# Kernel optimization log

Hardware: AMD Instinct MI355X
Metric: run time of the kernel (lower is better)

The kernel has to match this reference:

```python
import jax, jax.numpy as jnp
import numpy as np


def setup_inputs() -> dict:
    key = jax.random.key(0)
    k1, k2 = jax.random.split(key)
    inputs = jax.random.normal(k1, (16, 64, 64, 64), dtype=jnp.float32)  # NCHW, C=embedding_dim
    codebook = jax.random.normal(k2, (1024, 64), dtype=jnp.float32)      # [K, D]
    return {"inputs": inputs, "codebook": codebook}


def reference(inputs, codebook):
    # inputs: [B, C, H, W] -> [B, H, W, C] -> [N, D]
    D = codebook.shape[1]
    x = jnp.transpose(inputs, (0, 2, 3, 1)).reshape(-1, D)  # [N, D]
    distances = (
        jnp.sum(x * x, axis=1, keepdims=True)
        + jnp.sum(codebook * codebook, axis=1)
        - 2.0 * jnp.matmul(x, codebook.T)
    )
    encoding_indices = jnp.argmin(distances, axis=1)[:, None]  # [N, 1]
    return encoding_indices
```

## Files before the change

kernel.cpp:

```cpp
#include <hip/hip_runtime.h>


typedef float f4 __attribute__((ext_vector_type(4)));
typedef short s8v __attribute__((ext_vector_type(8)));
typedef unsigned int u32;

#define D_DIM 64
#define HW    4096
#define ROWS  64
#define INF_  __builtin_inff()
#define MFMA(a,b,c) __builtin_amdgcn_mfma_f32_16x16x32_bf16(a,b,c,0,0,0)

__device__ __forceinline__ unsigned short bf_rne(float f) {
    u32 u = __builtin_bit_cast(u32, f);
    u32 r = u + 0x7fffu + ((u >> 16) & 1u);
    return (unsigned short)(r >> 16);
}
__device__ __forceinline__ float bf_to_f(unsigned short h) {
    u32 u = ((u32)h) << 16;
    return __builtin_bit_cast(float, u);
}
__device__ __forceinline__ void split3(float f, unsigned short& h,
                                       unsigned short& m, unsigned short& l) {
    h = bf_rne(f);
    float f1 = f - bf_to_f(h);
    m = bf_rne(f1);
    float f2 = f1 - bf_to_f(m);
    l = bf_rne(f2);
}
__device__ __forceinline__ s8v pack8(unsigned short a0, unsigned short a1,
                                     unsigned short a2, unsigned short a3,
                                     unsigned short a4, unsigned short a5,
                                     unsigned short a6, unsigned short a7) {
    uint4 u;
    u.x = a0 | ((u32)a1 << 16);
    u.y = a2 | ((u32)a3 << 16);
    u.z = a4 | ((u32)a5 << 16);
    u.w = a6 | ((u32)a7 << 16);
    return __builtin_bit_cast(s8v, u);
}

__global__ __launch_bounds__(64) void prep_kernel(const float* __restrict__ cb,
                                                  char* __restrict__ wsb) {
    const int blk = blockIdx.x;
    const int lane = threadIdx.x;
    if (blk < 384) {
        const int T = blk / 6;
        const int rem = blk - T * 6;
        const int s = rem / 3;
        const int L = rem - s * 3;
        const int code = T * 16 + (lane & 15);
        const int ch0 = s * 32 + (lane >> 4) * 8;
        const float* src = cb + code * 64 + ch0;
        unsigned short o[8];
#pragma unroll
        for (int j = 0; j < 8; ++j) {
            unsigned short h, m2, l;
            split3(src[j], h, m2, l);
            o[j] = (L == 0) ? h : (L == 1) ? m2 : l;
        }
        uint4 w;
        w.x = o[0] | ((u32)o[1] << 16);
        w.y = o[2] | ((u32)o[3] << 16);
        w.z = o[4] | ((u32)o[5] << 16);
        w.w = o[6] | ((u32)o[7] << 16);
        *(uint4*)(wsb + (size_t)blk * 1024 + lane * 16) = w;
    } else {
        const int k = (blk - 384) * 64 + lane;
        const f4* row = (const f4*)(cb + (size_t)k * 64);
        float sacc = 0.f;
#pragma unroll
        for (int i = 0; i < 16; ++i) {
            f4 v = row[i];
            sacc = fmaf(v.x, v.x, sacc);
            sacc = fmaf(v.y, v.y, sacc);
            sacc = fmaf(v.z, v.z, sacc);
            sacc = fmaf(v.w, v.w, sacc);
        }
        ((float*)(wsb + 384 * 1024))[k] = sacc;
    }
}

#define BUILD_AS(rs, s) {                                                    \
    const float* xr = (const float*)&xs4[(rs) * 16 + m_][0];                 \
    f4 va = *(const f4*)(xr + (s) * 32 + ko);                                \
    f4 vb = *(const f4*)(xr + (s) * 32 + ko + 4);                            \
    unsigned short h0,h1,h2,h3,h4,h5,h6,h7;                                  \
    unsigned short q0,q1,q2,q3,q4,q5,q6,q7;                                  \
    unsigned short l0,l1,l2,l3,l4,l5,l6,l7;                                  \
    split3(-2.f * va.x, h0, q0, l0); split3(-2.f * va.y, h1, q1, l1);        \
    split3(-2.f * va.z, h2, q2, l2); split3(-2.f * va.w, h3, q3, l3);        \
    split3(-2.f * vb.x, h4, q4, l4); split3(-2.f * vb.y, h5, q5, l5);        \
    split3(-2.f * vb.z, h6, q6, l6); split3(-2.f * vb.w, h7, q7, l7);        \
    Ah##rs##s = pack8(h0,h1,h2,h3,h4,h5,h6,h7);                              \
    Am##rs##s = pack8(q0,q1,q2,q3,q4,q5,q6,q7);                              \
    Al##rs##s = pack8(l0,l1,l2,l3,l4,l5,l6,l7);                              \
}

#define LOADB(S, P)                                                          \
    Bh0##S = *(const s8v*)((P) + 0);    Bm0##S = *(const s8v*)((P) + 1024);  \
    Bl0##S = *(const s8v*)((P) + 2048); Bh1##S = *(const s8v*)((P) + 3072);  \
    Bm1##S = *(const s8v*)((P) + 4096); Bl1##S = *(const s8v*)((P) + 5120);

#define MFMA_S(s, BH, BM, BL)                                                \
    acc0 = MFMA(Ah0##s, BH, acc0); acc1 = MFMA(Ah1##s, BH, acc1);            \
    acc2 = MFMA(Ah2##s, BH, acc2); acc3 = MFMA(Ah3##s, BH, acc3);            \
    acc0 = MFMA(Ah0##s, BM, acc0); acc1 = MFMA(Ah1##s, BM, acc1);            \
    acc2 = MFMA(Ah2##s, BM, acc2); acc3 = MFMA(Ah3##s, BM, acc3);            \
    acc0 = MFMA(Am0##s, BH, acc0); acc1 = MFMA(Am1##s, BH, acc1);            \
    acc2 = MFMA(Am2##s, BH, acc2); acc3 = MFMA(Am3##s, BH, acc3);            \
    acc0 = MFMA(Ah0##s, BL, acc0); acc1 = MFMA(Ah1##s, BL, acc1);            \
    acc2 = MFMA(Ah2##s, BL, acc2); acc3 = MFMA(Ah3##s, BL, acc3);            \
    acc0 = MFMA(Am0##s, BM, acc0); acc1 = MFMA(Am1##s, BM, acc1);            \
    acc2 = MFMA(Am2##s, BM, acc2); acc3 = MFMA(Am3##s, BM, acc3);            \
    acc0 = MFMA(Al0##s, BH, acc0); acc1 = MFMA(Al1##s, BH, acc1);            \
    acc2 = MFMA(Al2##s, BH, acc2); acc3 = MFMA(Al3##s, BH, acc3);

#define UPD(rs, i) {                                                         \
    float v = acc##rs[i] + en;                                               \
    bool p = (v < best_##rs##_##i);                                          \
    best_##rs##_##i = p ? v : best_##rs##_##i;                               \
    idx_##rs##_##i  = p ? kn : idx_##rs##_##i;                               \
}
#define EPILOG(TG) {                                                         \
    const int kn = (TG) * 16 + m_;                                           \
    const float en = sEn[kn];                                                \
    UPD(0,0) UPD(0,1) UPD(0,2) UPD(0,3)                                      \
    UPD(1,0) UPD(1,1) UPD(1,2) UPD(1,3)                                      \
    UPD(2,0) UPD(2,1) UPD(2,2) UPD(2,3)                                      \
    UPD(3,0) UPD(3,1) UPD(3,2) UPD(3,3)                                      \
    acc0 = (f4){0.f,0.f,0.f,0.f}; acc1 = (f4){0.f,0.f,0.f,0.f};              \
    acc2 = (f4){0.f,0.f,0.f,0.f}; acc3 = (f4){0.f,0.f,0.f,0.f};              \
}

#define DO_TILE(CUR, NXT, TG, NP) {                                          \
    LOADB(NXT, NP)                                                           \
    MFMA_S(0, Bh0##CUR, Bm0##CUR, Bl0##CUR)                                  \
    MFMA_S(1, Bh1##CUR, Bm1##CUR, Bl1##CUR)                                  \
    EPILOG(TG)                                                               \
}

#define BFLY1(rs, i, msk) {                                                  \
    float ov = __shfl_xor(best_##rs##_##i, msk);                             \
    int   oi = __shfl_xor(idx_##rs##_##i,  msk);                             \
    bool p = (ov < best_##rs##_##i) ||                                       \
             (ov == best_##rs##_##i && oi < idx_##rs##_##i);                 \
    best_##rs##_##i = p ? ov : best_##rs##_##i;                              \
    idx_##rs##_##i  = p ? oi : idx_##rs##_##i;                               \
}
#define BFLY_ALL(msk)                                                        \
    BFLY1(0,0,msk) BFLY1(0,1,msk) BFLY1(0,2,msk) BFLY1(0,3,msk)              \
    BFLY1(1,0,msk) BFLY1(1,1,msk) BFLY1(1,2,msk) BFLY1(1,3,msk)              \
    BFLY1(2,0,msk) BFLY1(2,1,msk) BFLY1(2,2,msk) BFLY1(2,3,msk)              \
    BFLY1(3,0,msk) BFLY1(3,1,msk) BFLY1(3,2,msk) BFLY1(3,3,msk)

#define STORE1(rs, i)                                                        \
    sdq[quarter][(rs) * 16 + rbase + (i)] = best_##rs##_##i;                 \
    siq[quarter][(rs) * 16 + rbase + (i)] = idx_##rs##_##i;

__global__ __launch_bounds__(256, 2) void vq_kernel(const float* __restrict__ x,
                                                    const char* __restrict__ wsb,
                                                    int* __restrict__ out) {
    __shared__ f4    xs4[ROWS][17];
    __shared__ float sEn[1024];
    __shared__ float sdq[4][64];
    __shared__ int   siq[4][64];

    const int tid = threadIdx.x;
    const int lane = tid & 63;
    const int quarter = __builtin_amdgcn_readfirstlane(tid >> 6);
    const int m_ = lane & 15;
    const int ko = (lane >> 4) * 8;
    const int n0 = blockIdx.x * ROWS;
    const int b = n0 >> 12;
    const int hw0 = n0 & (HW - 1);

    const float* enp = (const float*)(wsb + 384 * 1024);
#pragma unroll
    for (int q = 0; q < 4; ++q) sEn[q * 256 + tid] = enp[q * 256 + tid];

    {
        const float* g = x + ((size_t)b * D_DIM + quarter * 16) * HW + hw0 + lane;
        float v[16];
#pragma unroll
        for (int i = 0; i < 16; ++i) v[i] = g[(size_t)i * HW];
#pragma unroll
        for (int j = 0; j < 4; ++j)
            xs4[lane][quarter * 4 + j] = (f4){v[4*j], v[4*j+1], v[4*j+2], v[4*j+3]};
    }
    __syncthreads();

    s8v Ah00, Am00, Al00, Ah01, Am01, Al01;
    s8v Ah10, Am10, Al10, Ah11, Am11, Al11;
    s8v Ah20, Am20, Al20, Ah21, Am21, Al21;
    s8v Ah30, Am30, Al30, Ah31, Am31, Al31;
    BUILD_AS(0,0) BUILD_AS(0,1) BUILD_AS(1,0) BUILD_AS(1,1)
    BUILD_AS(2,0) BUILD_AS(2,1) BUILD_AS(3,0) BUILD_AS(3,1)

    f4 acc0 = (f4){0.f,0.f,0.f,0.f}, acc1 = (f4){0.f,0.f,0.f,0.f};
    f4 acc2 = (f4){0.f,0.f,0.f,0.f}, acc3 = (f4){0.f,0.f,0.f,0.f};
    float best_0_0=INF_, best_0_1=INF_, best_0_2=INF_, best_0_3=INF_;
    float best_1_0=INF_, best_1_1=INF_, best_1_2=INF_, best_1_3=INF_;
    float best_2_0=INF_, best_2_1=INF_, best_2_2=INF_, best_2_3=INF_;
    float best_3_0=INF_, best_3_1=INF_, best_3_2=INF_, best_3_3=INF_;
    int idx_0_0=0, idx_0_1=0, idx_0_2=0, idx_0_3=0;
    int idx_1_0=0, idx_1_1=0, idx_1_2=0, idx_1_3=0;
    int idx_2_0=0, idx_2_1=0, idx_2_2=0, idx_2_3=0;
    int idx_3_0=0, idx_3_1=0, idx_3_2=0, idx_3_3=0;

    s8v Bh0c, Bm0c, Bl0c, Bh1c, Bm1c, Bl1c;
    s8v Bh0n, Bm0n, Bl0n, Bh1n, Bm1n, Bl1n;

    const char* const bp0 = wsb + (size_t)quarter * 98304 + (size_t)lane * 16;
    const char* bp = bp0;
    LOADB(c, bp)
    bp += 6144;

#pragma unroll 1
    for (int tt = 0; tt < 8; ++tt) {
        const int t0 = 2 * tt;
        DO_TILE(c, n, quarter * 16 + t0, bp)
        bp += 6144;
        const char* np = (tt == 7) ? bp0 : bp;
        DO_TILE(n, c, quarter * 16 + t0 + 1, np)
        bp += 6144;
    }

    BFLY_ALL(1) BFLY_ALL(2) BFLY_ALL(4) BFLY_ALL(8)

    if ((lane & 15) == 0) {
        const int rbase = (lane >> 4) * 4;
        STORE1(0,0) STORE1(0,1) STORE1(0,2) STORE1(0,3)
        STORE1(1,0) STORE1(1,1) STORE1(1,2) STORE1(1,3)
        STORE1(2,0) STORE1(2,1) STORE1(2,2) STORE1(2,3)
        STORE1(3,0) STORE1(3,1) STORE1(3,2) STORE1(3,3)
    }
    __syncthreads();

    if (tid < 64) {
        float bv = sdq[0][tid];
        int   bi = siq[0][tid];
#pragma unroll
        for (int q = 1; q < 4; ++q) {
            const float o = sdq[q][tid];
            const int  oi = siq[q][tid];
            if (o < bv) { bv = o; bi = oi; }
        }
        out[n0 + tid] = bi;
    }
}

extern "C" void kernel_launch(void* const* d_in, const int* in_sizes, int n_in,
                              void* d_out, int out_size, void* d_ws, size_t ws_size,
                              hipStream_t stream) {
    const float* x  = (const float*)d_in[0];
    const float* cb = (const float*)d_in[1];
    char* wsb = (char*)d_ws;
    int*  out = (int*)d_out;

    prep_kernel<<<dim3(400), dim3(64), 0, stream>>>(cb, wsb);
    vq_kernel<<<dim3(65536 / ROWS), dim3(256), 0, stream>>>(x, wsb, out);
}
```

Measured before the change: 110.4 us.

## Split rows across waves and stream codebook tiles through LDS with async loads

Each workgroup now handles 128 rows, and each wave owns 32 rows and scans the full codebook, instead of each wave owning a quarter of the codes for 64 shared rows. Codebook split tiles are staged into double-buffered LDS with global_load_lds, shared by all four waves, and synchronised with barriers. This removes the cross-wave argmin merge and cuts global B traffic per row. The costs are two barriers per tile and a serial dependency on the accumulators, since each accumulator now carries a chain of six MFMAs with only four independent chains. The grid is also halved.

Measured after the change: 110.6 us. About the same (+0.2%).

```diff
diff --git a/kernel.cpp b/kernel.cpp
--- a/kernel.cpp
+++ b/kernel.cpp
@@ -4,10 +4,12 @@
 typedef float f4 __attribute__((ext_vector_type(4)));
 typedef short s8v __attribute__((ext_vector_type(8)));
 typedef unsigned int u32;
+typedef __attribute__((address_space(1))) const u32* gas1;
+typedef __attribute__((address_space(3))) u32* las3;
 
 #define D_DIM 64
 #define HW    4096
-#define ROWS  64
+#define ROWS  128
 #define INF_  __builtin_inff()
 #define MFMA(a,b,c) __builtin_amdgcn_mfma_f32_16x16x32_bf16(a,b,c,0,0,0)
 
@@ -38,6 +40,9 @@
     u.z = a4 | ((u32)a5 << 16);
     u.w = a6 | ((u32)a7 << 16);
     return __builtin_bit_cast(s8v, u);
+}
+__device__ __forceinline__ void gl_lds16(const char* g, char* l) {
+    __builtin_amdgcn_global_load_lds((gas1)(const void*)g, (las3)(void*)l, 16, 0, 0);
 }
 
 __global__ __launch_bounds__(64) void prep_kernel(const float* __restrict__ cb,
@@ -82,7 +87,7 @@
 }
 
 #define BUILD_AS(rs, s) {                                                    \
-    const float* xr = (const float*)&xs4[(rs) * 16 + m_][0];                 \
+    const float* xr = (const float*)&xs4[wrow + (rs) * 16 + m_][0];          \
     f4 va = *(const f4*)(xr + (s) * 32 + ko);                                \
     f4 vb = *(const f4*)(xr + (s) * 32 + ko + 4);                            \
     unsigned short h0,h1,h2,h3,h4,h5,h6,h7;                                  \
@@ -97,47 +102,44 @@
     Al##rs##s = pack8(l0,l1,l2,l3,l4,l5,l6,l7);                              \
 }
 
-#define LOADB(S, P)                                                          \
-    Bh0##S = *(const s8v*)((P) + 0);    Bm0##S = *(const s8v*)((P) + 1024);  \
-    Bl0##S = *(const s8v*)((P) + 2048); Bh1##S = *(const s8v*)((P) + 3072);  \
-    Bm1##S = *(const s8v*)((P) + 4096); Bl1##S = *(const s8v*)((P) + 5120);
-
-#define MFMA_S(s, BH, BM, BL)                                                \
-    acc0 = MFMA(Ah0##s, BH, acc0); acc1 = MFMA(Ah1##s, BH, acc1);            \
-    acc2 = MFMA(Ah2##s, BH, acc2); acc3 = MFMA(Ah3##s, BH, acc3);            \
-    acc0 = MFMA(Ah0##s, BM, acc0); acc1 = MFMA(Ah1##s, BM, acc1);            \
-    acc2 = MFMA(Ah2##s, BM, acc2); acc3 = MFMA(Ah3##s, BM, acc3);            \
-    acc0 = MFMA(Am0##s, BH, acc0); acc1 = MFMA(Am1##s, BH, acc1);            \
-    acc2 = MFMA(Am2##s, BH, acc2); acc3 = MFMA(Am3##s, BH, acc3);            \
-    acc0 = MFMA(Ah0##s, BL, acc0); acc1 = MFMA(Ah1##s, BL, acc1);            \
-    acc2 = MFMA(Ah2##s, BL, acc2); acc3 = MFMA(Ah3##s, BL, acc3);            \
-    acc0 = MFMA(Am0##s, BM, acc0); acc1 = MFMA(Am1##s, BM, acc1);            \
-    acc2 = MFMA(Am2##s, BM, acc2); acc3 = MFMA(Am3##s, BM, acc3);            \
-    acc0 = MFMA(Al0##s, BH, acc0); acc1 = MFMA(Al1##s, BH, acc1);            \
-    acc2 = MFMA(Al2##s, BH, acc2); acc3 = MFMA(Al3##s, BH, acc3);
-
-#define UPD(rs, i) {                                                         \
-    float v = acc##rs[i] + en;                                               \
+#define STAGE(T, BUF) {                                                      \
+    const char* gs = wsb + (size_t)(T) * 6144 + lane16;                      \
+    gl_lds16(gs + quarter * 1024, (BUF) + quarter * 1024);                   \
+    if (quarter < 2)                                                         \
+        gl_lds16(gs + (4 + quarter) * 1024, (BUF) + (4 + quarter) * 1024);   \
+}
+
+#define READ6(LP)                                                            \
+    Bh0 = *(const s8v*)((LP) + 0);    Bm0 = *(const s8v*)((LP) + 1024);      \
+    Bl0 = *(const s8v*)((LP) + 2048); Bh1 = *(const s8v*)((LP) + 3072);      \
+    Bm1 = *(const s8v*)((LP) + 4096); Bl1 = *(const s8v*)((LP) + 5120);
+
+#define MTERM(AH, AM, AL, BH, BM, BL, ACC)                                   \
+    ACC = MFMA(AH, BH, ACC); ACC = MFMA(AH, BM, ACC);                        \
+    ACC = MFMA(AM, BH, ACC); ACC = MFMA(AH, BL, ACC);                        \
+    ACC = MFMA(AM, BM, ACC); ACC = MFMA(AL, BH, ACC);
+
+#define COMPUTE24()                                                          \
+    MTERM(Ah00, Am00, Al00, Bh0, Bm0, Bl0, a00)                              \
+    MTERM(Ah10, Am10, Al10, Bh0, Bm0, Bl0, a10)                              \
+    MTERM(Ah01, Am01, Al01, Bh1, Bm1, Bl1, a01)                              \
+    MTERM(Ah11, Am11, Al11, Bh1, Bm1, Bl1, a11)
+
+#define UPD(rs, i, SV) {                                                     \
+    float v = SV[i] + en;                                                    \
     bool p = (v < best_##rs##_##i);                                          \
     best_##rs##_##i = p ? v : best_##rs##_##i;                               \
     idx_##rs##_##i  = p ? kn : idx_##rs##_##i;                               \
 }
-#define EPILOG(TG) {                                                         \
-    const int kn = (TG) * 16 + m_;                                           \
+#define EPILOG(T) {                                                          \
+    const int kn = (T) * 16 + m_;                                            \
     const float en = sEn[kn];                                                \
-    UPD(0,0) UPD(0,1) UPD(0,2) UPD(0,3)                                      \
-    UPD(1,0) UPD(1,1) UPD(1,2) UPD(1,3)                                      \
-    UPD(2,0) UPD(2,1) UPD(2,2) UPD(2,3)                                      \
-    UPD(3,0) UPD(3,1) UPD(3,2) UPD(3,3)                                      \
-    acc0 = (f4){0.f,0.f,0.f,0.f}; acc1 = (f4){0.f,0.f,0.f,0.f};              \
-    acc2 = (f4){0.f,0.f,0.f,0.f}; acc3 = (f4){0.f,0.f,0.f,0.f};              \
-}
-
-#define DO_TILE(CUR, NXT, TG, NP) {                                          \
-    LOADB(NXT, NP)                                                           \
-    MFMA_S(0, Bh0##CUR, Bm0##CUR, Bl0##CUR)                                  \
-    MFMA_S(1, Bh1##CUR, Bm1##CUR, Bl1##CUR)                                  \
-    EPILOG(TG)                                                               \
+    f4 s0 = a00 + a01;                                                       \
+    f4 s1 = a10 + a11;                                                       \
+    UPD(0,0,s0) UPD(0,1,s0) UPD(0,2,s0) UPD(0,3,s0)                          \
+    UPD(1,0,s1) UPD(1,1,s1) UPD(1,2,s1) UPD(1,3,s1)                          \
+    a00 = (f4){0.f,0.f,0.f,0.f}; a01 = (f4){0.f,0.f,0.f,0.f};                \
+    a10 = (f4){0.f,0.f,0.f,0.f}; a11 = (f4){0.f,0.f,0.f,0.f};                \
 }
 
 #define BFLY1(rs, i, msk) {                                                  \
@@ -150,103 +152,93 @@
 }
 #define BFLY_ALL(msk)                                                        \
     BFLY1(0,0,msk) BFLY1(0,1,msk) BFLY1(0,2,msk) BFLY1(0,3,msk)              \
-    BFLY1(1,0,msk) BFLY1(1,1,msk) BFLY1(1,2,msk) BFLY1(1,3,msk)              \
-    BFLY1(2,0,msk) BFLY1(2,1,msk) BFLY1(2,2,msk) BFLY1(2,3,msk)              \
-    BFLY1(3,0,msk) BFLY1(3,1,msk) BFLY1(3,2,msk) BFLY1(3,3,msk)
-
-#define STORE1(rs, i)                                                        \
-    sdq[quarter][(rs) * 16 + rbase + (i)] = best_##rs##_##i;                 \
-    siq[quarter][(rs) * 16 + rbase + (i)] = idx_##rs##_##i;
+    BFLY1(1,0,msk) BFLY1(1,1,msk) BFLY1(1,2,msk) BFLY1(1,3,msk)
 
 __global__ __launch_bounds__(256, 2) void vq_kernel(const float* __restrict__ x,
                                                     const char* __restrict__ wsb,
                                                     int* __restrict__ out) {
-    __shared__ f4    xs4[ROWS][17];
+    __shared__ __align__(16) char LDSA[34816];
     __shared__ float sEn[1024];
-    __shared__ float sdq[4][64];
-    __shared__ int   siq[4][64];
 
     const int tid = threadIdx.x;
     const int lane = tid & 63;
     const int quarter = __builtin_amdgcn_readfirstlane(tid >> 6);
     const int m_ = lane & 15;
     const int ko = (lane >> 4) * 8;
+    const int lane16 = lane * 16;
+    const int wrow = quarter * 32;
     const int n0 = blockIdx.x * ROWS;
     const int b = n0 >> 12;
     const int hw0 = n0 & (HW - 1);
 
+    f4 (*xs4)[17] = (f4(*)[17])(void*)LDSA;
+    char* const buf0 = LDSA;
+    char* const buf1 = LDSA + 6144;
+
     const float* enp = (const float*)(wsb + 384 * 1024);
 #pragma unroll
     for (int q = 0; q < 4; ++q) sEn[q * 256 + tid] = enp[q * 256 + tid];
 
-    {
-        const float* g = x + ((size_t)b * D_DIM + quarter * 16) * HW + hw0 + lane;
+#pragma unroll
+    for (int pass = 0; pass < 2; ++pass) {
+        const int row = lane + pass * 64;
+        const float* g = x + ((size_t)b * D_DIM + quarter * 16) * HW + hw0 + row;
         float v[16];
 #pragma unroll
         for (int i = 0; i < 16; ++i) v[i] = g[(size_t)i * HW];
 #pragma unroll
         for (int j = 0; j < 4; ++j)
-            xs4[lane][quarter * 4 + j] = (f4){v[4*j], v[4*j+1], v[4*j+2], v[4*j+3]};
+            xs4[row][quarter * 4 + j] = (f4){v[4*j], v[4*j+1], v[4*j+2], v[4*j+3]};
     }
     __syncthreads();
 
     s8v Ah00, Am00, Al00, Ah01, Am01, Al01;
     s8v Ah10, Am10, Al10, Ah11, Am11, Al11;
-    s8v Ah20, Am20, Al20, Ah21, Am21, Al21;
-    s8v Ah30, Am30, Al30, Ah31, Am31, Al31;
     BUILD_AS(0,0) BUILD_AS(0,1) BUILD_AS(1,0) BUILD_AS(1,1)
-    BUILD_AS(2,0) BUILD_AS(2,1) BUILD_AS(3,0) BUILD_AS(3,1)
-
-    f4 acc0 = (f4){0.f,0.f,0.f,0.f}, acc1 = (f4){0.f,0.f,0.f,0.f};
-    f4 acc2 = (f4){0.f,0.f,0.f,0.f}, acc3 = (f4){0.f,0.f,0.f,0.f};
+    __syncthreads();
+
+    f4 a00 = (f4){0.f,0.f,0.f,0.f}, a01 = (f4){0.f,0.f,0.f,0.f};
+    f4 a10 = (f4){0.f,0.f,0.f,0.f}, a11 = (f4){0.f,0.f,0.f,0.f};
     float best_0_0=INF_, best_0_1=INF_, best_0_2=INF_, best_0_3=INF_;
     float best_1_0=INF_, best_1_1=INF_, best_1_2=INF_, best_1_3=INF_;
-    float best_2_0=INF_, best_2_1=INF_, best_2_2=INF_, best_2_3=INF_;
-    float best_3_0=INF_, best_3_1=INF_, best_3_2=INF_, best_3_3=INF_;
     int idx_0_0=0, idx_0_1=0, idx_0_2=0, idx_0_3=0;
     int idx_1_0=0, idx_1_1=0, idx_1_2=0, idx_1_3=0;
-    int idx_2_0=0, idx_2_1=0, idx_2_2=0, idx_2_3=0;
-    int idx_3_0=0, idx_3_1=0, idx_3_2=0, idx_3_3=0;
-
-    s8v Bh0c, Bm0c, Bl0c, Bh1c, Bm1c, Bl1c;
-    s8v Bh0n, Bm0n, Bl0n, Bh1n, Bm1n, Bl1n;
-
-    const char* const bp0 = wsb + (size_t)quarter * 98304 + (size_t)lane * 16;
-    const char* bp = bp0;
-    LOADB(c, bp)
-    bp += 6144;
+
+    s8v Bh0, Bm0, Bl0, Bh1, Bm1, Bl1;
+
+    STAGE(0, buf0)
+    __syncthreads();
 
 #pragma unroll 1
-    for (int tt = 0; tt < 8; ++tt) {
-        const int t0 = 2 * tt;
-        DO_TILE(c, n, quarter * 16 + t0, bp)
-        bp += 6144;
-        const char* np = (tt == 7) ? bp0 : bp;
-        DO_TILE(n, c, quarter * 16 + t0 + 1, np)
-        bp += 6144;
+    for (int tt = 0; tt < 32; ++tt) {
+        const int t = 2 * tt;
+        STAGE(t + 1, buf1)
+        READ6(buf0 + lane16)
+        COMPUTE24()
+        EPILOG(t)
+        __syncthreads();
+        if (tt != 31) STAGE(t + 2, buf0)
+        READ6(buf1 + lane16)
+        COMPUTE24()
+        EPILOG(t + 1)
+        __syncthreads();
     }
 
     BFLY_ALL(1) BFLY_ALL(2) BFLY_ALL(4) BFLY_ALL(8)
 
-    if ((lane & 15) == 0) {
+    if (m_ == 0) {
         const int rbase = (lane >> 4) * 4;
-        STORE1(0,0) STORE1(0,1) STORE1(0,2) STORE1(0,3)
-        STORE1(1,0) STORE1(1,1) STORE1(1,2) STORE1(1,3)
-        STORE1(2,0) STORE1(2,1) STORE1(2,2) STORE1(2,3)
-        STORE1(3,0) STORE1(3,1) STORE1(3,2) STORE1(3,3)
-    }
-    __syncthreads();
-
-    if (tid < 64) {
-        float bv = sdq[0][tid];
-        int   bi = siq[0][tid];
-#pragma unroll
-        for (int q = 1; q < 4; ++q) {
-            const float o = sdq[q][tid];
-            const int  oi = siq[q][tid];
-            if (o < bv) { bv = o; bi = oi; }
+#pragma unroll
+        for (int i = 0; i < 4; ++i) {
         }
-        out[n0 + tid] = bi;
+        out[n0 + wrow + 0 * 16 + rbase + 0] = idx_0_0;
+        out[n0 + wrow + 0 * 16 + rbase + 1] = idx_0_1;
+        out[n0 + wrow + 0 * 16 + rbase + 2] = idx_0_2;
+        out[n0 + wrow + 0 * 16 + rbase + 3] = idx_0_3;
+        out[n0 + wrow + 1 * 16 + rbase + 0] = idx_1_0;
+        out[n0 + wrow + 1 * 16 + rbase + 1] = idx_1_1;
+        out[n0 + wrow + 1 * 16 + rbase + 2] = idx_1_2;
+        out[n0 + wrow + 1 * 16 + rbase + 3] = idx_1_3;
     }
 }
 
```
